# Performance work log

Measured on AMD Instinct MI355X. Metric: run time of the kernel, lower is better.

The kernel has to match this reference:

```python
import jax, jax.numpy as jnp
import numpy as np


def setup_inputs() -> dict:
    key = jax.random.key(0)
    ks = jax.random.split(key, 6)
    B, S, D_IN, D_OUT = 4, 2048, 1024, 1024
    return {
        "inputs_for_keys": jax.random.normal(ks[0], (B, S, D_IN), dtype=jnp.float32),
        "inputs_for_values": jax.random.normal(ks[1], (B, S, D_IN), dtype=jnp.float32),
        "inputs_for_queries": jax.random.normal(ks[2], (B, S, D_IN), dtype=jnp.float32),
        "K_weight": jax.random.normal(ks[3], (D_IN, D_OUT), dtype=jnp.float32) * 0.1,
        "V_weight": jax.random.normal(ks[4], (D_IN, D_OUT), dtype=jnp.float32) * 0.1,
        "Q_weight": jax.random.normal(ks[5], (D_IN, D_OUT), dtype=jnp.float32) * 0.1,
    }


def reference(inputs_for_keys, inputs_for_values, inputs_for_queries,
              K_weight, V_weight, Q_weight):
    # QKV projections: [B,S,D_in] @ [D_in,D_out] -> [B,S,D_out]
    K = jnp.einsum("bsi,io->bso", inputs_for_keys, K_weight)
    V = jnp.einsum("bsi,io->bso", inputs_for_values, V_weight)
    Q = jnp.einsum("bsi,io->bso", inputs_for_queries, Q_weight)

    Sq, Sk, d = Q.shape[1], K.shape[1], K.shape[2]
    scale = 1.0 / jnp.sqrt(jnp.asarray(d, dtype=Q.dtype))
    # scaled dot-product scores: [B, Sq, Sk]
    scores = jnp.einsum("bqd,bkd->bqk", Q, K) * scale
    # causal mask: -inf strictly above the diagonal (key index > query index)
    causal = jnp.where(jnp.arange(Sk)[None, :] > jnp.arange(Sq)[:, None],
                       jnp.float32(-jnp.inf), jnp.float32(0.0))
    scores = scores + causal[None, :, :]
    probs = jax.nn.softmax(scores, axis=-1)
    return jnp.einsum("bqk,bkd->bqd", probs, V)
```

## Files before the change

### kernel.cpp

```cpp
#include <hip/hip_runtime.h>
#include <math.h>

using f32x4  = __attribute__((ext_vector_type(4))) float;
using f16x8  = __attribute__((ext_vector_type(8))) _Float16;
using u16x8  = __attribute__((ext_vector_type(8))) unsigned short;
using u16x4  = __attribute__((ext_vector_type(4))) unsigned short;

static __device__ __forceinline__ unsigned short f2h(float f) {
  _Float16 h = (_Float16)f;
  return __builtin_bit_cast(unsigned short, h);
}

static __device__ __forceinline__ f32x4 mfma_f16(f16x8 a, f16x8 b, f32x4 c) {
  return __builtin_amdgcn_mfma_f32_16x16x32_f16(a, b, c, 0, 0, 0);
}

static __device__ __forceinline__ void gll16(const void* g, void* l) {
  using GPtr = const unsigned int __attribute__((address_space(1)))*;
  using LPtr = unsigned int __attribute__((address_space(3)))*;
  __builtin_amdgcn_global_load_lds((GPtr)(unsigned long long)g,
                                   (LPtr)(unsigned)(unsigned long long)l,
                                   16, 0, 0);
}

static __device__ __forceinline__ void stage32(unsigned short* sdst,
                                               const unsigned short* g,
                                               size_t ld, int k0, int wave,
                                               int lane) {
  const int p = lane & 7, ll = lane >> 3;
#pragma unroll
  for (int i = 0; i < 2; ++i) {
    const int line = wave * 16 + i * 8 + ll;
    const int q = p ^ (line & 7);
    gll16(g + (size_t)(2 * line + (q >> 2)) * ld + (k0 + ((q & 3) << 3)),
          sdst + wave * 1024 + i * 512);
  }
}

static __device__ __forceinline__ f16x8 frag32(const unsigned short* s,
                                               int row, int kko) {
  const int line = row >> 1;
  const int q = ((row & 1) << 2) | (kko >> 3);
  const int p = q ^ (line & 7);
  return *(const f16x8*)&s[line * 64 + p * 8];
}

__global__ __launch_bounds__(256) void convert_wkq_kernel(
    const float* __restrict__ Wk, const float* __restrict__ Wq,
    unsigned short* __restrict__ Wkh, unsigned short* __restrict__ Wqh) {
  const int z = blockIdx.z;
  const float* W = z ? Wq : Wk;
  unsigned short* H = z ? Wqh : Wkh;
  const size_t base = (size_t)blockIdx.x * 4096 + threadIdx.x * 4;
  f32x4 v[4];
#pragma unroll
  for (int k = 0; k < 4; ++k) v[k] = *(const f32x4*)&W[base + k * 1024];
#pragma unroll
  for (int k = 0; k < 4; ++k) {
    u16x4 h;
#pragma unroll
    for (int e = 0; e < 4; ++e) h[e] = f2h(v[k][e]);
    *(u16x4*)&H[base + k * 1024] = h;
  }
}

__global__ __launch_bounds__(256) void convert_wv_kernel(
    const float* __restrict__ Wv, unsigned short* __restrict__ WvT) {
  __shared__ float sW[64][65];
  const int ti = blockIdx.x * 64;
  const int tj = blockIdx.y * 64;
  const int tid = threadIdx.x;
#pragma unroll
  for (int it = 0; it < 4; ++it) {
    int idx = tid + it * 256;
    int r = idx >> 4, c = (idx & 15) << 2;
    f32x4 v = *(const f32x4*)&Wv[(size_t)(ti + r) * 1024 + tj + c];
    sW[r][c] = v[0]; sW[r][c + 1] = v[1]; sW[r][c + 2] = v[2]; sW[r][c + 3] = v[3];
  }
  __syncthreads();
#pragma unroll
  for (int it = 0; it < 4; ++it) {
    int idx = tid + it * 256;
    int ro = idx >> 4, ci = (idx & 15) << 2;
    u16x4 h;
#pragma unroll
    for (int e = 0; e < 4; ++e) h[e] = f2h(sW[ci + e][ro]);
    *(u16x4*)&WvT[(size_t)(tj + ro) * 1024 + ti + ci] = h;
  }
}

__global__ __launch_bounds__(256) void convert_x_kernel(
    const float* __restrict__ Xk, const float* __restrict__ Xq,
    const float* __restrict__ Xv, unsigned short* __restrict__ Xkh,
    unsigned short* __restrict__ Xqh, unsigned short* __restrict__ Xvh) {
  const int z = blockIdx.z;
  const float* X = (z == 0) ? Xk : (z == 1) ? Xq : Xv;
  unsigned short* H = (z == 0) ? Xkh : (z == 1) ? Xqh : Xvh;
  const size_t base = (size_t)blockIdx.x * 4096 + threadIdx.x * 4;
  f32x4 v[4];
#pragma unroll
  for (int k = 0; k < 4; ++k) v[k] = *(const f32x4*)&X[base + k * 1024];
#pragma unroll
  for (int k = 0; k < 4; ++k) {
    u16x4 h;
#pragma unroll
    for (int e = 0; e < 4; ++e) h[e] = f2h(v[k][e]);
    *(u16x4*)&H[base + k * 1024] = h;
  }
}

template <int EPI, bool PACKED, bool PVK>
__global__ __launch_bounds__(256, 4) void gemm_db_kernel(
    const unsigned short* __restrict__ Ah, const unsigned short* __restrict__ Bh,
    size_t lda, size_t ldb, int K,
    float* __restrict__ Cf, unsigned short* __restrict__ Ch, size_t ldc,
    size_t abatch, size_t bbatch, size_t cbatch) {
  constexpr int TILE = 128 * 32;
  __shared__ unsigned short smem[2][2 * TILE];

  int lid = blockIdx.x + gridDim.x * (blockIdx.y + gridDim.y * blockIdx.z);
  {
    const int n = gridDim.x * gridDim.y * gridDim.z;
    const int q = n >> 3, r = n & 7, x = lid & 7, k = lid >> 3;
    lid = (x < r ? x * (q + 1) : r * (q + 1) + (x - r) * q) + k;
  }
  int bm, bn, b;
  if constexpr (PACKED) {
    const int t = lid % gridDim.x;
    b = lid / gridDim.x;
    bm = (int)((sqrtf(8.f * (float)t + 1.f) - 1.f) * 0.5f);
    while ((bm + 1) * (bm + 2) / 2 <= t) ++bm;
    while (bm * (bm + 1) / 2 > t) --bm;
    bn = t - bm * (bm + 1) / 2;
  } else {
    bn = lid % gridDim.x;
    const int tmp = lid / gridDim.x;
    bm = tmp % gridDim.y;
    b = tmp / gridDim.y;
    if constexpr (PVK) bm = (int)gridDim.y - 1 - bm;
  }
  const int tid = threadIdx.x, lane = tid & 63, wave = tid >> 6;
  const unsigned short* gA = Ah + abatch * b + (size_t)(bm * 128) * lda;
  const unsigned short* gB = Bh + bbatch * b + (size_t)(bn * 128) * ldb;
  const int kend = PVK ? (bm + 1) * 128 : K;
  const int nsteps = kend / 32;
  f32x4 acc[4][4] = {};
  const int wr = (wave >> 1) << 6, wc = (wave & 1) << 6;
  const int frow = lane & 15, koff = (lane >> 4) << 3;

  auto stage_all = [&](unsigned short* buf, int k0) {
    stage32(buf, gA, lda, k0, wave, lane);
    stage32(buf + TILE, gB, ldb, k0, wave, lane);
  };

  stage_all(smem[0], 0);
  if (nsteps > 1) stage_all(smem[1], 32);
  int cur = 0;
  for (int st = 0; st < nsteps; ++st) {
    if (st + 1 < nsteps) {
      asm volatile("s_waitcnt vmcnt(4)" ::: "memory");
    } else {
      asm volatile("s_waitcnt vmcnt(0)" ::: "memory");
    }
    __builtin_amdgcn_sched_barrier(0);
    __builtin_amdgcn_s_barrier();
    __builtin_amdgcn_sched_barrier(0);
    const unsigned short* sA = smem[cur];
    const unsigned short* sB = smem[cur] + TILE;
    f16x8 fB[4];
#pragma unroll
    for (int j = 0; j < 4; ++j) fB[j] = frag32(sB, wc + j * 16 + frow, koff);
#pragma unroll
    for (int i = 0; i < 4; ++i) {
      const f16x8 a = frag32(sA, wr + i * 16 + frow, koff);
#pragma unroll
      for (int j = 0; j < 4; ++j) acc[i][j] = mfma_f16(a, fB[j], acc[i][j]);
    }
    asm volatile("s_waitcnt lgkmcnt(0)" ::: "memory");
    __builtin_amdgcn_sched_barrier(0);
    __builtin_amdgcn_s_barrier();
    __builtin_amdgcn_sched_barrier(0);
    if (st + 2 < nsteps) stage_all(smem[cur], (st + 2) * 32);
    cur ^= 1;
  }

  const int erow = bm * 128 + wr + ((lane >> 4) << 2);
  const int ecol = bn * 128 + wc + frow;
  if constexpr (EPI == 0) {
    float* C = Cf + cbatch * b;
#pragma unroll
    for (int i = 0; i < 4; ++i)
#pragma unroll
      for (int j = 0; j < 4; ++j)
#pragma unroll
        for (int e = 0; e < 4; ++e)
          C[(size_t)(erow + i * 16 + e) * ldc + (ecol + j * 16)] = acc[i][j][e];
  } else if constexpr (EPI == 3) {
#pragma unroll
    for (int i = 0; i < 4; ++i)
#pragma unroll
      for (int j = 0; j < 4; ++j) {
        const int s = erow + i * 16;
        const int o = ecol + j * 16;
        u16x4 v;
#pragma unroll
        for (int e = 0; e < 4; ++e) v[e] = f2h(acc[i][j][e]);
        *(u16x4*)&Ch[((size_t)(s >> 11) * 1024 + o) * 2048 + (s & 2047)] = v;
      }
  } else {
    unsigned short* Cho = Ch + cbatch * b;
#pragma unroll
    for (int i = 0; i < 4; ++i)
#pragma unroll
      for (int j = 0; j < 4; ++j)
#pragma unroll
        for (int e = 0; e < 4; ++e)
          Cho[(size_t)(erow + i * 16 + e) * ldc + (ecol + j * 16)] =
              f2h(acc[i][j][e]);
  }
}

__global__ __launch_bounds__(256) void reduce_mt_kernel(
    const float* __restrict__ P, unsigned short* __restrict__ H) {
  const size_t base = ((size_t)blockIdx.x * 256 + threadIdx.x) * 4;
  f32x4 s = *(const f32x4*)&P[base];
#pragma unroll
  for (int z = 1; z < 4; ++z) {
    f32x4 v = *(const f32x4*)&P[(size_t)z * 1048576 + base];
    s[0] += v[0]; s[1] += v[1]; s[2] += v[2]; s[3] += v[3];
  }
  u16x4 h;
#pragma unroll
  for (int e = 0; e < 4; ++e) h[e] = f2h(s[e]);
  *(u16x4*)&H[base] = h;
}

__global__ __launch_bounds__(256) void softmax_kernel(float* __restrict__ Sc) {
  const int row = blockIdx.x;
  const int q = row & 2047;
  const int tid = threadIdx.x, lane = tid & 63, wave = tid >> 6;
  float* srow = Sc + (size_t)row * 2048;
  unsigned short* prow = (unsigned short*)srow;
  const int k0 = tid * 4, k1 = 1024 + tid * 4;
  f32x4 v0 = {}, v1 = {};
  if (k0 <= q) v0 = *(const f32x4*)(srow + k0);
  if (k1 <= q) v1 = *(const f32x4*)(srow + k1);
  float m = -3.0e38f;
#pragma unroll
  for (int e = 0; e < 4; ++e) {
    if (k0 + e <= q) m = fmaxf(m, v0[e]);
    if (k1 + e <= q) m = fmaxf(m, v1[e]);
  }
#pragma unroll
  for (int o = 32; o; o >>= 1) m = fmaxf(m, __shfl_xor(m, o));
  __shared__ float redm[4], reds[4];
  if (lane == 0) redm[wave] = m;
  __syncthreads();
  m = fmaxf(fmaxf(redm[0], redm[1]), fmaxf(redm[2], redm[3]));
  const float scale = 0.03125f;
  float p[8];
  float s = 0.f;
#pragma unroll
  for (int e = 0; e < 4; ++e) {
    p[e] = (k0 + e <= q) ? __expf((v0[e] - m) * scale) : 0.f;
    p[4 + e] = (k1 + e <= q) ? __expf((v1[e] - m) * scale) : 0.f;
    s += p[e] + p[4 + e];
  }
#pragma unroll
  for (int o = 32; o; o >>= 1) s += __shfl_xor(s, o);
  if (lane == 0) reds[wave] = s;
  __syncthreads();
  s = reds[0] + reds[1] + reds[2] + reds[3];
  const float inv = 1.0f / s;
  u16x4 o0, o1;
#pragma unroll
  for (int e = 0; e < 4; ++e) {
    o0[e] = f2h(p[e] * inv);
    o1[e] = f2h(p[4 + e] * inv);
  }
  *(u16x4*)&prow[k0] = o0;
  *(u16x4*)&prow[k1] = o1;
}

extern "C" void kernel_launch(void* const* d_in, const int* in_sizes, int n_in,
                              void* d_out, int out_size, void* d_ws, size_t ws_size,
                              hipStream_t stream) {
  const float* Xk = (const float*)d_in[0];
  const float* Xv = (const float*)d_in[1];
  const float* Xq = (const float*)d_in[2];
  const float* Wk = (const float*)d_in[3];
  const float* Wv = (const float*)d_in[4];
  const float* Wq = (const float*)d_in[5];
  float* out = (float*)d_out;

  char* ws = (char*)d_ws;
  const size_t MB = 1024ull * 1024;
  unsigned short* Xqh   = (unsigned short*)(ws + 0);
  unsigned short* Xvh   = (unsigned short*)(ws + 16 * MB);
  unsigned short* Wkh   = (unsigned short*)(ws + 32 * MB);
  unsigned short* Wqh   = (unsigned short*)(ws + 34 * MB);
  unsigned short* MTh   = (unsigned short*)(ws + 40 * MB);
  unsigned short* WvT   = (unsigned short*)(ws + 44 * MB);
  float*          MTpart= (float*)(ws + 46 * MB);
  unsigned short* Xkh   = (unsigned short*)(ws + 64 * MB);
  unsigned short* Th    = (unsigned short*)(ws + 80 * MB);
  unsigned short* VT    = (unsigned short*)(ws + 96 * MB);
  float*          Sc    = (float*)(ws + 0);

  convert_wkq_kernel<<<dim3(256, 1, 2), 256, 0, stream>>>(Wk, Wq, Wkh, Wqh);
  convert_wv_kernel<<<dim3(16, 16), 256, 0, stream>>>(Wv, WvT);
  convert_x_kernel<<<dim3(2048, 1, 3), 256, 0, stream>>>(Xk, Xq, Xv, Xkh, Xqh, Xvh);

  gemm_db_kernel<0, false, false><<<dim3(8, 8, 4), 256, 0, stream>>>(
      Wkh, Wqh, 1024, 1024, 256, MTpart, nullptr, 1024, 256, 256,
      (size_t)1024 * 1024);
  reduce_mt_kernel<<<dim3(1024), 256, 0, stream>>>(MTpart, MTh);

  gemm_db_kernel<2, false, false><<<dim3(8, 64, 1), 256, 0, stream>>>(
      Xqh, MTh, 1024, 1024, 1024, nullptr, Th, 1024, 0, 0, 0);

  gemm_db_kernel<3, false, false><<<dim3(8, 64, 1), 256, 0, stream>>>(
      Xvh, WvT, 1024, 1024, 1024, nullptr, VT, 2048, 0, 0, 0);

  gemm_db_kernel<0, true, false><<<dim3(136, 1, 4), 256, 0, stream>>>(
      Th, Xkh, 1024, 1024, 1024, Sc, nullptr, 2048, (size_t)2048 * 1024,
      (size_t)2048 * 1024, (size_t)2048 * 2048);

  softmax_kernel<<<dim3(8192), 256, 0, stream>>>(Sc);

  gemm_db_kernel<0, false, true><<<dim3(8, 16, 4), 256, 0, stream>>>(
      (const unsigned short*)Sc, VT, 4096, 2048, 2048, out, nullptr, 1024,
      (size_t)2048 * 4096, (size_t)1024 * 2048, (size_t)2048 * 1024);
}
```

Measured before the change: 177.0 us.

## Fuse fp32-to-fp16 conversion of Xq/Xv into projection GEMMs; widen K-tile to 64

Drops the standalone conversion of the query and value inputs. A new GEMM variant stages the fp32 activations directly into LDS and converts them to fp16 while loading fragments, which removes a full write and re-read of two 16 MB half-precision buffers. The generic GEMM's K step also doubles from 32 to 64 with a new swizzled layout, and its occupancy hint drops to 2. The fused kernel reads twice the A bytes per tile and does conversion ALU work in the inner loop, and the larger LDS footprint lowers occupancy.

```diff
diff --git a/kernel.cpp b/kernel.cpp
--- a/kernel.cpp
+++ b/kernel.cpp
@@ -23,10 +23,26 @@
                                    16, 0, 0);
 }
 
-static __device__ __forceinline__ void stage32(unsigned short* sdst,
-                                               const unsigned short* g,
-                                               size_t ld, int k0, int wave,
-                                               int lane) {
+static __device__ __forceinline__ void stage64h(unsigned short* sdst,
+                                                const unsigned short* g,
+                                                size_t ld, int k0, int wave,
+                                                int lane) {
+  const int r = lane >> 3, c8 = lane & 7;
+  const int scol = (c8 ^ r) << 3;
+#pragma unroll
+  for (int i = 0; i < 4; ++i)
+    gll16(g + (size_t)(wave * 32 + i * 8 + r) * ld + (k0 + scol),
+          sdst + wave * 2048 + i * 512);
+}
+static __device__ __forceinline__ f16x8 frag64h(const unsigned short* s,
+                                                int row, int kko) {
+  return *(const f16x8*)&s[row * 64 + (kko ^ ((row & 7) << 3))];
+}
+
+static __device__ __forceinline__ void stage32h(unsigned short* sdst,
+                                                const unsigned short* g,
+                                                size_t ld, int k0, int wave,
+                                                int lane) {
   const int p = lane & 7, ll = lane >> 3;
 #pragma unroll
   for (int i = 0; i < 2; ++i) {
@@ -36,13 +52,38 @@
           sdst + wave * 1024 + i * 512);
   }
 }
-
-static __device__ __forceinline__ f16x8 frag32(const unsigned short* s,
-                                               int row, int kko) {
+static __device__ __forceinline__ f16x8 frag32h(const unsigned short* s,
+                                                int row, int kko) {
   const int line = row >> 1;
   const int q = ((row & 1) << 2) | (kko >> 3);
   const int p = q ^ (line & 7);
   return *(const f16x8*)&s[line * 64 + p * 8];
+}
+
+static __device__ __forceinline__ void stage32f(float* dst, const float* g,
+                                                size_t ld, int k0, int wave,
+                                                int lane) {
+  const int c8 = lane & 7, lr = lane >> 3;
+#pragma unroll
+  for (int i = 0; i < 4; ++i) {
+    const int row = wave * 32 + i * 8 + lr;
+    const int q = c8 ^ (row & 7);
+    gll16(g + (size_t)row * ld + (k0 + (q << 2)), dst + wave * 1024 + i * 256);
+  }
+}
+static __device__ __forceinline__ f16x8 frag32f(const float* s, int row,
+                                                int koff) {
+  const int r7 = row & 7;
+  const int q0 = koff >> 2;
+  f32x4 lo = *(const f32x4*)&s[row * 32 + ((q0 ^ r7) << 2)];
+  f32x4 hi = *(const f32x4*)&s[row * 32 + (((q0 + 1) ^ r7) << 2)];
+  f16x8 o;
+#pragma unroll
+  for (int e = 0; e < 4; ++e) {
+    o[e] = (_Float16)lo[e];
+    o[4 + e] = (_Float16)hi[e];
+  }
+  return o;
 }
 
 __global__ __launch_bounds__(256) void convert_wkq_kernel(
@@ -89,33 +130,28 @@
   }
 }
 
-__global__ __launch_bounds__(256) void convert_x_kernel(
-    const float* __restrict__ Xk, const float* __restrict__ Xq,
-    const float* __restrict__ Xv, unsigned short* __restrict__ Xkh,
-    unsigned short* __restrict__ Xqh, unsigned short* __restrict__ Xvh) {
-  const int z = blockIdx.z;
-  const float* X = (z == 0) ? Xk : (z == 1) ? Xq : Xv;
-  unsigned short* H = (z == 0) ? Xkh : (z == 1) ? Xqh : Xvh;
+__global__ __launch_bounds__(256) void convert_xk_kernel(
+    const float* __restrict__ Xk, unsigned short* __restrict__ Xkh) {
   const size_t base = (size_t)blockIdx.x * 4096 + threadIdx.x * 4;
   f32x4 v[4];
 #pragma unroll
-  for (int k = 0; k < 4; ++k) v[k] = *(const f32x4*)&X[base + k * 1024];
+  for (int k = 0; k < 4; ++k) v[k] = *(const f32x4*)&Xk[base + k * 1024];
 #pragma unroll
   for (int k = 0; k < 4; ++k) {
     u16x4 h;
 #pragma unroll
     for (int e = 0; e < 4; ++e) h[e] = f2h(v[k][e]);
-    *(u16x4*)&H[base + k * 1024] = h;
+    *(u16x4*)&Xkh[base + k * 1024] = h;
   }
 }
 
 template <int EPI, bool PACKED, bool PVK>
-__global__ __launch_bounds__(256, 4) void gemm_db_kernel(
+__global__ __launch_bounds__(256, 2) void gemm_db_kernel(
     const unsigned short* __restrict__ Ah, const unsigned short* __restrict__ Bh,
     size_t lda, size_t ldb, int K,
     float* __restrict__ Cf, unsigned short* __restrict__ Ch, size_t ldc,
     size_t abatch, size_t bbatch, size_t cbatch) {
-  constexpr int TILE = 128 * 32;
+  constexpr int TILE = 128 * 64;
   __shared__ unsigned short smem[2][2 * TILE];
 
   int lid = blockIdx.x + gridDim.x * (blockIdx.y + gridDim.y * blockIdx.z);
@@ -143,22 +179,22 @@
   const unsigned short* gA = Ah + abatch * b + (size_t)(bm * 128) * lda;
   const unsigned short* gB = Bh + bbatch * b + (size_t)(bn * 128) * ldb;
   const int kend = PVK ? (bm + 1) * 128 : K;
-  const int nsteps = kend / 32;
+  const int nsteps = kend / 64;
   f32x4 acc[4][4] = {};
   const int wr = (wave >> 1) << 6, wc = (wave & 1) << 6;
   const int frow = lane & 15, koff = (lane >> 4) << 3;
 
   auto stage_all = [&](unsigned short* buf, int k0) {
-    stage32(buf, gA, lda, k0, wave, lane);
-    stage32(buf + TILE, gB, ldb, k0, wave, lane);
+    stage64h(buf, gA, lda, k0, wave, lane);
+    stage64h(buf + TILE, gB, ldb, k0, wave, lane);
   };
 
   stage_all(smem[0], 0);
-  if (nsteps > 1) stage_all(smem[1], 32);
+  if (nsteps > 1) stage_all(smem[1], 64);
   int cur = 0;
   for (int st = 0; st < nsteps; ++st) {
     if (st + 1 < nsteps) {
-      asm volatile("s_waitcnt vmcnt(4)" ::: "memory");
+      asm volatile("s_waitcnt vmcnt(8)" ::: "memory");
     } else {
       asm volatile("s_waitcnt vmcnt(0)" ::: "memory");
     }
@@ -167,20 +203,24 @@
     __builtin_amdgcn_sched_barrier(0);
     const unsigned short* sA = smem[cur];
     const unsigned short* sB = smem[cur] + TILE;
-    f16x8 fB[4];
-#pragma unroll
-    for (int j = 0; j < 4; ++j) fB[j] = frag32(sB, wc + j * 16 + frow, koff);
-#pragma unroll
-    for (int i = 0; i < 4; ++i) {
-      const f16x8 a = frag32(sA, wr + i * 16 + frow, koff);
-#pragma unroll
-      for (int j = 0; j < 4; ++j) acc[i][j] = mfma_f16(a, fB[j], acc[i][j]);
+#pragma unroll
+    for (int kk = 0; kk < 64; kk += 32) {
+      const int kko = kk + koff;
+      f16x8 fB[4];
+#pragma unroll
+      for (int j = 0; j < 4; ++j) fB[j] = frag64h(sB, wc + j * 16 + frow, kko);
+#pragma unroll
+      for (int i = 0; i < 4; ++i) {
+        const f16x8 a = frag64h(sA, wr + i * 16 + frow, kko);
+#pragma unroll
+        for (int j = 0; j < 4; ++j) acc[i][j] = mfma_f16(a, fB[j], acc[i][j]);
+      }
     }
     asm volatile("s_waitcnt lgkmcnt(0)" ::: "memory");
     __builtin_amdgcn_sched_barrier(0);
     __builtin_amdgcn_s_barrier();
     __builtin_amdgcn_sched_barrier(0);
-    if (st + 2 < nsteps) stage_all(smem[cur], (st + 2) * 32);
+    if (st + 2 < nsteps) stage_all(smem[cur], (st + 2) * 64);
     cur ^= 1;
   }
 
@@ -195,7 +235,80 @@
 #pragma unroll
         for (int e = 0; e < 4; ++e)
           C[(size_t)(erow + i * 16 + e) * ldc + (ecol + j * 16)] = acc[i][j][e];
-  } else if constexpr (EPI == 3) {
+  } else {
+    unsigned short* Cho = Ch + cbatch * b;
+#pragma unroll
+    for (int i = 0; i < 4; ++i)
+#pragma unroll
+      for (int j = 0; j < 4; ++j)
+#pragma unroll
+        for (int e = 0; e < 4; ++e)
+          Cho[(size_t)(erow + i * 16 + e) * ldc + (ecol + j * 16)] =
+              f2h(acc[i][j][e]);
+  }
+}
+
+template <int EPI>
+__global__ __launch_bounds__(256, 3) void gemm_cvta_kernel(
+    const float* __restrict__ Af, const unsigned short* __restrict__ Bh,
+    size_t lda, size_t ldb, int K, unsigned short* __restrict__ Ch,
+    size_t ldc) {
+  __shared__ float sA[2][128 * 32];
+  __shared__ unsigned short sB[2][128 * 32];
+
+  int lid = blockIdx.x + gridDim.x * blockIdx.y;
+  {
+    const int n = gridDim.x * gridDim.y;
+    const int q = n >> 3, r = n & 7, x = lid & 7, k = lid >> 3;
+    lid = (x < r ? x * (q + 1) : r * (q + 1) + (x - r) * q) + k;
+  }
+  const int bn = lid % gridDim.x;
+  const int bm = lid / gridDim.x;
+  const int tid = threadIdx.x, lane = tid & 63, wave = tid >> 6;
+  const float* gA = Af + (size_t)(bm * 128) * lda;
+  const unsigned short* gB = Bh + (size_t)(bn * 128) * ldb;
+  const int nsteps = K / 32;
+  f32x4 acc[4][4] = {};
+  const int wr = (wave >> 1) << 6, wc = (wave & 1) << 6;
+  const int frow = lane & 15, koff = (lane >> 4) << 3;
+
+  auto stage_all = [&](int buf, int k0) {
+    stage32f(sA[buf], gA, lda, k0, wave, lane);
+    stage32h(sB[buf], gB, ldb, k0, wave, lane);
+  };
+
+  stage_all(0, 0);
+  stage_all(1, 32);
+  int cur = 0;
+  for (int st = 0; st < nsteps; ++st) {
+    if (st + 1 < nsteps) {
+      asm volatile("s_waitcnt vmcnt(6)" ::: "memory");
+    } else {
+      asm volatile("s_waitcnt vmcnt(0)" ::: "memory");
+    }
+    __builtin_amdgcn_sched_barrier(0);
+    __builtin_amdgcn_s_barrier();
+    __builtin_amdgcn_sched_barrier(0);
+    f16x8 fB[4];
+#pragma unroll
+    for (int j = 0; j < 4; ++j) fB[j] = frag32h(sB[cur], wc + j * 16 + frow, koff);
+#pragma unroll
+    for (int i = 0; i < 4; ++i) {
+      const f16x8 a = frag32f(sA[cur], wr + i * 16 + frow, koff);
+#pragma unroll
+      for (int j = 0; j < 4; ++j) acc[i][j] = mfma_f16(a, fB[j], acc[i][j]);
+    }
+    asm volatile("s_waitcnt lgkmcnt(0)" ::: "memory");
+    __builtin_amdgcn_sched_barrier(0);
+    __builtin_amdgcn_s_barrier();
+    __builtin_amdgcn_sched_barrier(0);
+    if (st + 2 < nsteps) stage_all(cur, (st + 2) * 32);
+    cur ^= 1;
+  }
+
+  const int erow = bm * 128 + wr + ((lane >> 4) << 2);
+  const int ecol = bn * 128 + wc + frow;
+  if constexpr (EPI == 3) {
 #pragma unroll
     for (int i = 0; i < 4; ++i)
 #pragma unroll
@@ -208,14 +321,13 @@
         *(u16x4*)&Ch[((size_t)(s >> 11) * 1024 + o) * 2048 + (s & 2047)] = v;
       }
   } else {
-    unsigned short* Cho = Ch + cbatch * b;
 #pragma unroll
     for (int i = 0; i < 4; ++i)
 #pragma unroll
       for (int j = 0; j < 4; ++j)
 #pragma unroll
         for (int e = 0; e < 4; ++e)
-          Cho[(size_t)(erow + i * 16 + e) * ldc + (ecol + j * 16)] =
+          Ch[(size_t)(erow + i * 16 + e) * ldc + (ecol + j * 16)] =
               f2h(acc[i][j][e]);
   }
 }
@@ -295,32 +407,30 @@
 
   char* ws = (char*)d_ws;
   const size_t MB = 1024ull * 1024;
-  unsigned short* Xqh   = (unsigned short*)(ws + 0);
-  unsigned short* Xvh   = (unsigned short*)(ws + 16 * MB);
-  unsigned short* Wkh   = (unsigned short*)(ws + 32 * MB);
-  unsigned short* Wqh   = (unsigned short*)(ws + 34 * MB);
-  unsigned short* MTh   = (unsigned short*)(ws + 40 * MB);
-  unsigned short* WvT   = (unsigned short*)(ws + 44 * MB);
-  float*          MTpart= (float*)(ws + 46 * MB);
+  float*          Sc    = (float*)(ws + 0);
   unsigned short* Xkh   = (unsigned short*)(ws + 64 * MB);
   unsigned short* Th    = (unsigned short*)(ws + 80 * MB);
   unsigned short* VT    = (unsigned short*)(ws + 96 * MB);
-  float*          Sc    = (float*)(ws + 0);
+  unsigned short* MTh   = (unsigned short*)(ws + 112 * MB);
+  unsigned short* Wkh   = (unsigned short*)(ws + 114 * MB);
+  unsigned short* Wqh   = (unsigned short*)(ws + 116 * MB);
+  unsigned short* WvT   = (unsigned short*)(ws + 118 * MB);
+  float*          MTpart= (float*)(ws + 120 * MB);
 
   convert_wkq_kernel<<<dim3(256, 1, 2), 256, 0, stream>>>(Wk, Wq, Wkh, Wqh);
   convert_wv_kernel<<<dim3(16, 16), 256, 0, stream>>>(Wv, WvT);
-  convert_x_kernel<<<dim3(2048, 1, 3), 256, 0, stream>>>(Xk, Xq, Xv, Xkh, Xqh, Xvh);
+  convert_xk_kernel<<<dim3(2048), 256, 0, stream>>>(Xk, Xkh);
 
   gemm_db_kernel<0, false, false><<<dim3(8, 8, 4), 256, 0, stream>>>(
       Wkh, Wqh, 1024, 1024, 256, MTpart, nullptr, 1024, 256, 256,
       (size_t)1024 * 1024);
   reduce_mt_kernel<<<dim3(1024), 256, 0, stream>>>(MTpart, MTh);
 
-  gemm_db_kernel<2, false, false><<<dim3(8, 64, 1), 256, 0, stream>>>(
-      Xqh, MTh, 1024, 1024, 1024, nullptr, Th, 1024, 0, 0, 0);
-
-  gemm_db_kernel<3, false, false><<<dim3(8, 64, 1), 256, 0, stream>>>(
-      Xvh, WvT, 1024, 1024, 1024, nullptr, VT, 2048, 0, 0, 0);
+  gemm_cvta_kernel<2><<<dim3(8, 64), 256, 0, stream>>>(
+      Xq, MTh, 1024, 1024, 1024, Th, 1024);
+
+  gemm_cvta_kernel<3><<<dim3(8, 64), 256, 0, stream>>>(
+      Xv, WvT, 1024, 1024, 1024, VT, 2048);
 
   gemm_db_kernel<0, true, false><<<dim3(136, 1, 4), 256, 0, stream>>>(
       Th, Xkh, 1024, 1024, 1024, Sc, nullptr, 2048, (size_t)2048 * 1024,
```

Measured after the change: 176.4 us. About the same (-0.4%).

## Double GEMM K-tile to 64 with XOR-swizzled LDS and separate compact P buffer

Applied to the files above, without the earlier changes.

The GEMM kernel now stages 64-wide K tiles per step instead of 32, using a new row-wise XOR swizzle for LDS stores and fragment loads. Occupancy drops from 4 to 2 blocks per SM because LDS use doubles, and the wait count changes to match. Softmax now writes fp16 probabilities into a separate dense buffer with leading dimension 2048, and only up to the causal block boundary. The PV GEMM then reads that contiguous buffer rather than the aliased strided fp32 score rows. The aim is to halve barrier and loop overhead per K element and to improve P locality, at the cost of more LDS per block and lower occupancy.

```diff
diff --git a/kernel.cpp b/kernel.cpp
--- a/kernel.cpp
+++ b/kernel.cpp
@@ -23,26 +23,20 @@
                                    16, 0, 0);
 }
 
-static __device__ __forceinline__ void stage32(unsigned short* sdst,
-                                               const unsigned short* g,
-                                               size_t ld, int k0, int wave,
-                                               int lane) {
-  const int p = lane & 7, ll = lane >> 3;
-#pragma unroll
-  for (int i = 0; i < 2; ++i) {
-    const int line = wave * 16 + i * 8 + ll;
-    const int q = p ^ (line & 7);
-    gll16(g + (size_t)(2 * line + (q >> 2)) * ld + (k0 + ((q & 3) << 3)),
-          sdst + wave * 1024 + i * 512);
-  }
-}
-
-static __device__ __forceinline__ f16x8 frag32(const unsigned short* s,
-                                               int row, int kko) {
-  const int line = row >> 1;
-  const int q = ((row & 1) << 2) | (kko >> 3);
-  const int p = q ^ (line & 7);
-  return *(const f16x8*)&s[line * 64 + p * 8];
+static __device__ __forceinline__ void stage64h(unsigned short* sdst,
+                                                const unsigned short* g,
+                                                size_t ld, int k0, int wave,
+                                                int lane) {
+  const int r = lane >> 3, c8 = lane & 7;
+  const int scol = (c8 ^ r) << 3;
+#pragma unroll
+  for (int i = 0; i < 4; ++i)
+    gll16(g + (size_t)(wave * 32 + i * 8 + r) * ld + (k0 + scol),
+          sdst + wave * 2048 + i * 512);
+}
+static __device__ __forceinline__ f16x8 frag64h(const unsigned short* s,
+                                                int row, int kko) {
+  return *(const f16x8*)&s[row * 64 + (kko ^ ((row & 7) << 3))];
 }
 
 __global__ __launch_bounds__(256) void convert_wkq_kernel(
@@ -110,12 +104,12 @@
 }
 
 template <int EPI, bool PACKED, bool PVK>
-__global__ __launch_bounds__(256, 4) void gemm_db_kernel(
+__global__ __launch_bounds__(256, 2) void gemm_db_kernel(
     const unsigned short* __restrict__ Ah, const unsigned short* __restrict__ Bh,
     size_t lda, size_t ldb, int K,
     float* __restrict__ Cf, unsigned short* __restrict__ Ch, size_t ldc,
     size_t abatch, size_t bbatch, size_t cbatch) {
-  constexpr int TILE = 128 * 32;
+  constexpr int TILE = 128 * 64;
   __shared__ unsigned short smem[2][2 * TILE];
 
   int lid = blockIdx.x + gridDim.x * (blockIdx.y + gridDim.y * blockIdx.z);
@@ -143,22 +137,22 @@
   const unsigned short* gA = Ah + abatch * b + (size_t)(bm * 128) * lda;
   const unsigned short* gB = Bh + bbatch * b + (size_t)(bn * 128) * ldb;
   const int kend = PVK ? (bm + 1) * 128 : K;
-  const int nsteps = kend / 32;
+  const int nsteps = kend / 64;
   f32x4 acc[4][4] = {};
   const int wr = (wave >> 1) << 6, wc = (wave & 1) << 6;
   const int frow = lane & 15, koff = (lane >> 4) << 3;
 
   auto stage_all = [&](unsigned short* buf, int k0) {
-    stage32(buf, gA, lda, k0, wave, lane);
-    stage32(buf + TILE, gB, ldb, k0, wave, lane);
+    stage64h(buf, gA, lda, k0, wave, lane);
+    stage64h(buf + TILE, gB, ldb, k0, wave, lane);
   };
 
   stage_all(smem[0], 0);
-  if (nsteps > 1) stage_all(smem[1], 32);
+  if (nsteps > 1) stage_all(smem[1], 64);
   int cur = 0;
   for (int st = 0; st < nsteps; ++st) {
     if (st + 1 < nsteps) {
-      asm volatile("s_waitcnt vmcnt(4)" ::: "memory");
+      asm volatile("s_waitcnt vmcnt(8)" ::: "memory");
     } else {
       asm volatile("s_waitcnt vmcnt(0)" ::: "memory");
     }
@@ -167,20 +161,24 @@
     __builtin_amdgcn_sched_barrier(0);
     const unsigned short* sA = smem[cur];
     const unsigned short* sB = smem[cur] + TILE;
-    f16x8 fB[4];
-#pragma unroll
-    for (int j = 0; j < 4; ++j) fB[j] = frag32(sB, wc + j * 16 + frow, koff);
-#pragma unroll
-    for (int i = 0; i < 4; ++i) {
-      const f16x8 a = frag32(sA, wr + i * 16 + frow, koff);
-#pragma unroll
-      for (int j = 0; j < 4; ++j) acc[i][j] = mfma_f16(a, fB[j], acc[i][j]);
+#pragma unroll
+    for (int kk = 0; kk < 64; kk += 32) {
+      const int kko = kk + koff;
+      f16x8 fB[4];
+#pragma unroll
+      for (int j = 0; j < 4; ++j) fB[j] = frag64h(sB, wc + j * 16 + frow, kko);
+#pragma unroll
+      for (int i = 0; i < 4; ++i) {
+        const f16x8 a = frag64h(sA, wr + i * 16 + frow, kko);
+#pragma unroll
+        for (int j = 0; j < 4; ++j) acc[i][j] = mfma_f16(a, fB[j], acc[i][j]);
+      }
     }
     asm volatile("s_waitcnt lgkmcnt(0)" ::: "memory");
     __builtin_amdgcn_sched_barrier(0);
     __builtin_amdgcn_s_barrier();
     __builtin_amdgcn_sched_barrier(0);
-    if (st + 2 < nsteps) stage_all(smem[cur], (st + 2) * 32);
+    if (st + 2 < nsteps) stage_all(smem[cur], (st + 2) * 64);
     cur ^= 1;
   }
 
@@ -235,12 +233,14 @@
   *(u16x4*)&H[base] = h;
 }
 
-__global__ __launch_bounds__(256) void softmax_kernel(float* __restrict__ Sc) {
+__global__ __launch_bounds__(256) void softmax_kernel(
+    const float* __restrict__ Sc, unsigned short* __restrict__ P) {
   const int row = blockIdx.x;
   const int q = row & 2047;
+  const int kendr = ((q >> 7) + 1) << 7;
   const int tid = threadIdx.x, lane = tid & 63, wave = tid >> 6;
-  float* srow = Sc + (size_t)row * 2048;
-  unsigned short* prow = (unsigned short*)srow;
+  const float* srow = Sc + (size_t)row * 2048;
+  unsigned short* prow = P + (size_t)row * 2048;
   const int k0 = tid * 4, k1 = 1024 + tid * 4;
   f32x4 v0 = {}, v1 = {};
   if (k0 <= q) v0 = *(const f32x4*)(srow + k0);
@@ -272,14 +272,18 @@
   __syncthreads();
   s = reds[0] + reds[1] + reds[2] + reds[3];
   const float inv = 1.0f / s;
-  u16x4 o0, o1;
-#pragma unroll
-  for (int e = 0; e < 4; ++e) {
-    o0[e] = f2h(p[e] * inv);
-    o1[e] = f2h(p[4 + e] * inv);
-  }
-  *(u16x4*)&prow[k0] = o0;
-  *(u16x4*)&prow[k1] = o1;
+  if (k0 < kendr) {
+    u16x4 o0;
+#pragma unroll
+    for (int e = 0; e < 4; ++e) o0[e] = f2h(p[e] * inv);
+    *(u16x4*)&prow[k0] = o0;
+  }
+  if (k1 < kendr) {
+    u16x4 o1;
+#pragma unroll
+    for (int e = 0; e < 4; ++e) o1[e] = f2h(p[4 + e] * inv);
+    *(u16x4*)&prow[k1] = o1;
+  }
 }
 
 extern "C" void kernel_launch(void* const* d_in, const int* in_sizes, int n_in,
@@ -295,17 +299,19 @@
 
   char* ws = (char*)d_ws;
   const size_t MB = 1024ull * 1024;
-  unsigned short* Xqh   = (unsigned short*)(ws + 0);
-  unsigned short* Xvh   = (unsigned short*)(ws + 16 * MB);
-  unsigned short* Wkh   = (unsigned short*)(ws + 32 * MB);
-  unsigned short* Wqh   = (unsigned short*)(ws + 34 * MB);
-  unsigned short* MTh   = (unsigned short*)(ws + 40 * MB);
-  unsigned short* WvT   = (unsigned short*)(ws + 44 * MB);
-  float*          MTpart= (float*)(ws + 46 * MB);
+  float*          Sc    = (float*)(ws + 0);
   unsigned short* Xkh   = (unsigned short*)(ws + 64 * MB);
-  unsigned short* Th    = (unsigned short*)(ws + 80 * MB);
-  unsigned short* VT    = (unsigned short*)(ws + 96 * MB);
-  float*          Sc    = (float*)(ws + 0);
+  unsigned short* Xqh   = (unsigned short*)(ws + 80 * MB);
+  unsigned short* Xvh   = (unsigned short*)(ws + 96 * MB);
+  unsigned short* Th    = (unsigned short*)(ws + 112 * MB);
+  unsigned short* VT    = (unsigned short*)(ws + 128 * MB);
+  unsigned short* MTh   = (unsigned short*)(ws + 144 * MB);
+  unsigned short* Wkh   = (unsigned short*)(ws + 146 * MB);
+  unsigned short* Wqh   = (unsigned short*)(ws + 148 * MB);
+  unsigned short* WvT   = (unsigned short*)(ws + 150 * MB);
+  float*          MTpart= (float*)(ws + 152 * MB);
+  unsigned short* Pd    = (unsigned short*)(ws + 0);
+  Pd = (unsigned short*)(ws + 168 * MB);
 
   convert_wkq_kernel<<<dim3(256, 1, 2), 256, 0, stream>>>(Wk, Wq, Wkh, Wqh);
   convert_wv_kernel<<<dim3(16, 16), 256, 0, stream>>>(Wv, WvT);
@@ -326,9 +332,9 @@
       Th, Xkh, 1024, 1024, 1024, Sc, nullptr, 2048, (size_t)2048 * 1024,
       (size_t)2048 * 1024, (size_t)2048 * 2048);
 
-  softmax_kernel<<<dim3(8192), 256, 0, stream>>>(Sc);
+  softmax_kernel<<<dim3(8192), 256, 0, stream>>>(Sc, Pd);
 
   gemm_db_kernel<0, false, true><<<dim3(8, 16, 4), 256, 0, stream>>>(
-      (const unsigned short*)Sc, VT, 4096, 2048, 2048, out, nullptr, 1024,
-      (size_t)2048 * 4096, (size_t)1024 * 2048, (size_t)2048 * 1024);
-}
+      Pd, VT, 2048, 2048, 2048, out, nullptr, 1024,
+      (size_t)2048 * 2048, (size_t)1024 * 2048, (size_t)2048 * 1024);
+}
```

Result: faster. 166.2 us (-6.1%).
